# Kernel optimization log

Hardware: AMD Instinct MI355X
Metric: run time of the kernel (lower is better)

The kernel has to match this reference:

```python
import jax, jax.numpy as jnp
import numpy as np

L = 2        # num_layers (also acts as GRU seq_len due to the reshape in the original)
H = 512      # decoder_hidden_dim
Z = 512      # z_dim
V = 50257    # vocab_dim
T = 128      # target_length (max_length)
SOS_INDEX = 0


def setup_inputs() -> dict:
    key = jax.random.key(0)
    ks = jax.random.split(key, 16)
    def rn(k, shape, s=0.05):
        return jax.random.normal(k, shape, dtype=jnp.float32) * s
    input_variable = jax.random.normal(ks[0], (L, 1, Z), dtype=jnp.float32)
    tgt_idx = jax.random.randint(ks[1], (T,), 0, V)
    target_variable = jax.nn.one_hot(tgt_idx, V, dtype=jnp.float32).reshape(T, 1, V)
    sos = jax.nn.one_hot(jnp.array([SOS_INDEX]), V, dtype=jnp.float32)  # [1, V]
    return dict(
        input_variable=input_variable,
        target_variable=target_variable,
        sos=sos,
        emb_W=rn(ks[2], (L * H, V)), emb_b=rn(ks[3], (L * H,)),
        W_ih0=rn(ks[4], (3 * H, Z + H)), W_hh0=rn(ks[5], (3 * H, H)),
        b_ih0=rn(ks[6], (3 * H,)), b_hh0=rn(ks[7], (3 * H,)),
        W_ih1=rn(ks[8], (3 * H, H)), W_hh1=rn(ks[9], (3 * H, H)),
        b_ih1=rn(ks[10], (3 * H,)), b_hh1=rn(ks[11], (3 * H,)),
        out_W=rn(ks[12], (V, H)), out_b=rn(ks[13], (V,)),
    )


def _gru_cell(x, h, W_ih, W_hh, b_ih, b_hh):
    # PyTorch GRU cell semantics.
    gi = x @ W_ih.T + b_ih              # [1, 3H]
    gh = h @ W_hh.T + b_hh              # [1, 3H]
    i_r, i_z, i_n = jnp.split(gi, 3, axis=-1)
    h_r, h_z, h_n = jnp.split(gh, 3, axis=-1)
    r = jax.nn.sigmoid(i_r + h_r)
    z = jax.nn.sigmoid(i_z + h_z)
    n = jnp.tanh(i_n + r * h_n)
    return (1.0 - z) * n + z * h


def reference(input_variable, target_variable, sos,
              emb_W, emb_b,
              W_ih0, W_hh0, b_ih0, b_hh0,
              W_ih1, W_hh1, b_ih1, b_hh1,
              out_W, out_b):
    Wih = [W_ih0, W_ih1]; Whh = [W_hh0, W_hh1]
    bih = [b_ih0, b_ih1]; bhh = [b_hh0, b_hh1]

    def step(carry, tgt_t):
        hidden, inp = carry                      # hidden [L,1,H], inp [1,V]
        emb = jax.nn.relu((inp @ emb_W.T + emb_b).reshape(L, 1, H))
        layer_in = jnp.concatenate([input_variable, emb], axis=2)  # [L,1,Z+H]
        h_new = []
        for l in range(L):                       # GRU layers
            h = hidden[l]                        # [1,H]
            outs = []
            for t in range(L):                   # GRU 'time' steps (== L by construction)
                h = _gru_cell(layer_in[t], h, Wih[l], Whh[l], bih[l], bhh[l])
                outs.append(h)
            layer_in = jnp.stack(outs)           # [L,1,H]
            h_new.append(h)
        probs = jax.nn.softmax(layer_in[0] @ out_W.T + out_b, axis=1)  # [1,V]
        return (jnp.stack(h_new), tgt_t), probs[0]

    hidden0 = jnp.zeros((L, 1, H), jnp.float32)
    _, probs = jax.lax.scan(step, (hidden0, sos), target_variable)  # [T,V]
    idxs = jnp.argmax(probs, axis=-1)            # decoder_idxs
    return probs, idxs
```

## Files before the change

kernel.cpp:

```cpp
#include <hip/hip_runtime.h>
#include <math.h>

#define HD 512
#define VD 50257
#define TD 128
#define NB6 786

#define OFF_EMB     0u
#define OFF_X0      131072u
#define OFF_OUTS0   524288u
#define OFF_O       655360u
#define OFF_BASE    720896u
#define OFF_IDX     723968u
#define OFF_H0      724096u
#define OFF_H1      725120u
#define OFF_FLAGS   726144u
#define OFF_PM      729216u
#define OFF_PMPART  729472u
#define OFF_SUMS    930688u

__global__ void k_zero(float* p, int n){
  int i = blockIdx.x*256 + threadIdx.x;
  if (i < n) p[i] = 0.f;
}

__global__ void k_idx(const float* __restrict__ tgt, const float* __restrict__ sos,
                      int* __restrict__ idx){
  int t = blockIdx.x;
  const float* src = (t == 0) ? sos : (tgt + (size_t)(t-1)*VD);
  for (int v = threadIdx.x; v < VD; v += 256)
    if (src[v] > 0.5f) idx[t] = v;
}

__global__ void k_emb(const float* __restrict__ embW, const float* __restrict__ embB,
                      const int* __restrict__ idx, float* __restrict__ emb){
  int t = blockIdx.x;
  int j = blockIdx.y*256 + threadIdx.x;
  float v = embW[(size_t)j*VD + idx[t]] + embB[j];
  emb[t*1024 + j] = v > 0.f ? v : 0.f;
}

__global__ void k_base(const float* __restrict__ Wih0, const float* __restrict__ bih0,
                       const float* __restrict__ iv, float* __restrict__ base){
  int wave = threadIdx.x >> 6, lane = threadIdx.x & 63;
  int o = blockIdx.x*4 + wave;
  int tt = o / 1536, r = o % 1536;
  float s = 0.f;
  for (int c = lane; c < HD; c += 64)
    s += Wih0[(size_t)r*1024 + c] * iv[tt*HD + c];
  for (int off = 32; off; off >>= 1) s += __shfl_xor(s, off);
  if (lane == 0) base[o] = bih0[r] + s;
}

__global__ __launch_bounds__(256) void k_x0(const float* __restrict__ Wih0,
    const float* __restrict__ emb, const float* __restrict__ base, float* __restrict__ X0){
  __shared__ float Wt[64*33];
  __shared__ float Et[64*33];
  int tid = threadIdx.x;
  int r0 = blockIdx.x*64, b0 = blockIdx.y*64;
  int tx = tid & 15, ty = tid >> 4;
  float acc[4][4];
  #pragma unroll
  for (int i=0;i<4;i++)
    #pragma unroll
    for (int j=0;j<4;j++) acc[i][j] = 0.f;
  int lr = tid >> 2, lk = (tid & 3) * 8;
  for (int kk = 0; kk < HD; kk += 32){
    __syncthreads();
    {
      const float4* wg = (const float4*)(Wih0 + (size_t)(r0+lr)*1024 + HD + kk + lk);
      float4 a = wg[0], b = wg[1];
      float* d = Wt + lr*33 + lk;
      d[0]=a.x; d[1]=a.y; d[2]=a.z; d[3]=a.w; d[4]=b.x; d[5]=b.y; d[6]=b.z; d[7]=b.w;
    }
    {
      int bb = b0 + lr; int te = bb >> 1, hf = bb & 1;
      const float4* eg = (const float4*)(emb + (size_t)te*1024 + hf*HD + kk + lk);
      float4 a = eg[0], b = eg[1];
      float* d = Et + lr*33 + lk;
      d[0]=a.x; d[1]=a.y; d[2]=a.z; d[3]=a.w; d[4]=b.x; d[5]=b.y; d[6]=b.z; d[7]=b.w;
    }
    __syncthreads();
    #pragma unroll
    for (int k=0;k<32;k++){
      float wv[4], ev[4];
      #pragma unroll
      for (int i=0;i<4;i++) wv[i] = Wt[(tx*4+i)*33 + k];
      #pragma unroll
      for (int j=0;j<4;j++) ev[j] = Et[(ty*4+j)*33 + k];
      #pragma unroll
      for (int i=0;i<4;i++)
        #pragma unroll
        for (int j=0;j<4;j++) acc[i][j] += wv[i]*ev[j];
    }
  }
  #pragma unroll
  for (int j=0;j<4;j++){
    int bb = b0 + ty*4 + j;
    #pragma unroll
    for (int i=0;i<4;i++){
      int r = r0 + tx*4 + i;
      X0[(size_t)bb*1536 + r] = acc[i][j] + base[(bb&1)*1536 + r];
    }
  }
}

__device__ __forceinline__ void wait_flags(unsigned int* base, int n, unsigned int target, int tid){
  if (tid < 64){
    long iter = 0;
    for (;;){
      unsigned int v = 0;
      if (tid < n)
        v = __hip_atomic_load(base + tid*32, __ATOMIC_ACQUIRE, __HIP_MEMORY_SCOPE_AGENT);
      bool ok = (tid >= n) || (v >= target);
      if (__all((int)ok)) break;
      __builtin_amdgcn_s_sleep(1);
      if (++iter > 2000000L) break;
    }
  }
  __syncthreads();
}

__global__ __launch_bounds__(256, 1) void k_chain(
    const float* __restrict__ Whh0, const float* __restrict__ Wih1, const float* __restrict__ Whh1,
    const float* __restrict__ bhh0, const float* __restrict__ bih1, const float* __restrict__ bhh1,
    const float* __restrict__ X0, float* __restrict__ outs0, float* __restrict__ o,
    float* h0, float* h1, unsigned int* flags)
{
  const int w = blockIdx.x, tid = threadIdx.x;
  const bool isA = (w < 32);
  __shared__ float red[64];
  float wreg[128];
  const int sub = tid & 3;
  int slot; bool act;
  const float* wsrc = nullptr;
  if (isA){
    int ul = tid >> 4;
    int q  = (tid >> 2) & 3;
    int u  = w*16 + ul;
    slot = q; act = (q < 3);
    if (act) wsrc = Whh0 + ((size_t)(q*HD + u)*HD + sub*128);
  } else {
    int wp = w - 32;
    int ul = tid >> 5;
    int s8 = (tid >> 2) & 7;
    int u  = wp*8 + ul;
    slot = s8; act = (s8 < 6);
    if (s8 < 3)      wsrc = Wih1 + ((size_t)(s8*HD + u)*HD + sub*128);
    else if (s8 < 6) wsrc = Whh1 + ((size_t)((s8-3)*HD + u)*HD + sub*128);
  }
  if (wsrc){
    #pragma unroll
    for (int i=0;i<128;i++) wreg[i] = wsrc[i];
  } else {
    #pragma unroll
    for (int i=0;i<128;i++) wreg[i] = 0.f;
  }
  const int nGate = isA ? 16 : 8;
  float gb0=0,gb1=0,gb2=0,gb3=0,gb4=0,gb5=0;
  if (tid < nGate){
    int ug = isA ? (w*16 + tid) : ((w-32)*8 + tid);
    if (isA){ gb0=bhh0[ug]; gb1=bhh0[HD+ug]; gb2=bhh0[2*HD+ug]; }
    else {    gb0=bih1[ug]; gb1=bih1[HD+ug]; gb2=bih1[2*HD+ug];
              gb3=bhh1[ug]; gb4=bhh1[HD+ug]; gb5=bhh1[2*HD+ug]; }
  }
  unsigned int* flagsA = flags;
  unsigned int* flagsB = flags + 32*32;

  for (int c = 0; c < 256; c++){
    if (!isA) wait_flags(flagsA, 32, (unsigned)(c+1), tid);
    float partial = 0.f;
    if (act){
      const float* xp;
      if (isA) xp = h0 + (c&1)*HD + sub*128;
      else xp = (slot < 3) ? (outs0 + c*HD + sub*128) : (h1 + (c&1)*HD + sub*128);
      const float4* x4 = (const float4*)xp;
      #pragma unroll
      for (int i=0;i<32;i++){
        float4 xv = x4[i];
        partial += wreg[4*i]*xv.x + wreg[4*i+1]*xv.y + wreg[4*i+2]*xv.z + wreg[4*i+3]*xv.w;
      }
    }
    partial += __shfl_xor(partial, 1);
    partial += __shfl_xor(partial, 2);
    if (act && sub == 0){
      if (isA) red[(tid>>4)*4 + slot] = partial;
      else     red[(tid>>5)*8 + slot] = partial;
    }
    __syncthreads();
    if (tid < nGate){
      int ug = isA ? (w*16 + tid) : ((w-32)*8 + tid);
      float ir, iz, in_, hr, hz, hn;
      if (isA){
        const float* xo = X0 + (size_t)c*1536;
        ir = xo[ug]; iz = xo[HD+ug]; in_ = xo[2*HD+ug];
        hr = red[tid*4+0] + gb0; hz = red[tid*4+1] + gb1; hn = red[tid*4+2] + gb2;
      } else {
        ir = red[tid*8+0] + gb0; iz = red[tid*8+1] + gb1; in_ = red[tid*8+2] + gb2;
        hr = red[tid*8+3] + gb3; hz = red[tid*8+4] + gb4; hn = red[tid*8+5] + gb5;
      }
      float* hb = isA ? h0 : h1;
      float hprev = hb[(c&1)*HD + ug];
      float r = 1.f/(1.f + expf(-(ir+hr)));
      float z = 1.f/(1.f + expf(-(iz+hz)));
      float n = tanhf(in_ + r*hn);
      float hnew = (1.f - z)*n + z*hprev;
      hb[((c+1)&1)*HD + ug] = hnew;
      if (isA) outs0[c*HD + ug] = hnew;
      else if ((c & 1) == 0) o[(c>>1)*HD + ug] = hnew;
    }
    __syncthreads();
    if (tid == 0){
      unsigned int* myflag = isA ? (flagsA + w*32) : (flagsB + (w-32)*32);
      __hip_atomic_store(myflag, (unsigned)(c+1), __ATOMIC_RELEASE, __HIP_MEMORY_SCOPE_AGENT);
    }
    if (isA) wait_flags(flagsA, 32, (unsigned)(c+1), tid);
    else     wait_flags(flagsB, 64, (unsigned)(c+1), tid);
  }
}

__global__ __launch_bounds__(256) void k_logits(const float* __restrict__ o,
    const float* __restrict__ outW, const float* __restrict__ outB,
    float* __restrict__ dout, unsigned long long* __restrict__ pm_part){
  __shared__ float os[128*66];
  __shared__ float wsld[64*66];
  int tid = threadIdx.x;
  int v0 = blockIdx.x * 64;
  float acc[8][4];
  #pragma unroll
  for (int i=0;i<8;i++)
    #pragma unroll
    for (int j=0;j<4;j++) acc[i][j] = 0.f;
  int tx = tid & 15, ty = tid >> 4;
  for (int kk = 0; kk < HD; kk += 64){
    __syncthreads();
    {
      int tloc = tid >> 1, k0 = (tid & 1) * 32;
      const float4* og = (const float4*)(o + (size_t)tloc*HD + kk + k0);
      #pragma unroll
      for (int q=0;q<8;q++){
        float4 x = og[q]; int kb = k0 + q*4;
        os[tloc*66+kb]=x.x; os[tloc*66+kb+1]=x.y; os[tloc*66+kb+2]=x.z; os[tloc*66+kb+3]=x.w;
      }
    }
    {
      int vloc = tid >> 2, k0 = (tid & 3) * 16;
      int v = v0 + vloc;
      if (v < VD){
        const float4* wg = (const float4*)(outW + (size_t)v*HD + kk + k0);
        #pragma unroll
        for (int q=0;q<4;q++){
          float4 x = wg[q]; int kb = k0 + q*4;
          wsld[vloc*66+kb]=x.x; wsld[vloc*66+kb+1]=x.y; wsld[vloc*66+kb+2]=x.z; wsld[vloc*66+kb+3]=x.w;
        }
      } else {
        #pragma unroll
        for (int q=0;q<16;q++) wsld[vloc*66+k0+q] = 0.f;
      }
    }
    __syncthreads();
    #pragma unroll 8
    for (int k=0;k<64;k++){
      float ov[8], wv[4];
      #pragma unroll
      for (int i=0;i<8;i++) ov[i] = os[(tx*8+i)*66 + k];
      #pragma unroll
      for (int j=0;j<4;j++) wv[j] = wsld[(ty*4+j)*66 + k];
      #pragma unroll
      for (int i=0;i<8;i++)
        #pragma unroll
        for (int j=0;j<4;j++) acc[i][j] += ov[i]*wv[j];
    }
  }
  __syncthreads();
  unsigned long long* cand = (unsigned long long*)wsld;
  float bias[4]; int vj[4];
  #pragma unroll
  for (int j=0;j<4;j++){
    vj[j] = v0 + ty*4 + j;
    bias[j] = (vj[j] < VD) ? outB[vj[j]] : 0.f;
  }
  #pragma unroll
  for (int i=0;i<8;i++){
    int t = tx*8 + i;
    unsigned long long best = 0ull;
    #pragma unroll
    for (int j=0;j<4;j++){
      if (vj[j] < VD){
        float lg = acc[i][j] + bias[j];
        dout[(size_t)t*VD + vj[j]] = lg;
        unsigned b = __float_as_uint(lg);
        unsigned key = (b & 0x80000000u) ? ~b : (b | 0x80000000u);
        unsigned long long p = ((unsigned long long)key << 32) | (unsigned long long)(~(unsigned)vj[j]);
        if (p > best) best = p;
      }
    }
    cand[t*16 + ty] = best;
  }
  __syncthreads();
  if (tid < 128){
    unsigned long long best = 0ull;
    #pragma unroll
    for (int y=0;y<16;y++){
      unsigned long long p = cand[tid*16 + y];
      if (p > best) best = p;
    }
    pm_part[(size_t)tid*NB6 + blockIdx.x] = best;
  }
}

__global__ void k_pmred(const unsigned long long* __restrict__ pm_part,
                        unsigned long long* __restrict__ pm){
  int t = blockIdx.x, tid = threadIdx.x;
  __shared__ unsigned long long s[256];
  unsigned long long best = 0ull;
  for (int i = tid; i < NB6; i += 256){
    unsigned long long p = pm_part[(size_t)t*NB6 + i];
    if (p > best) best = p;
  }
  s[tid] = best; __syncthreads();
  for (int st = 128; st; st >>= 1){
    if (tid < st){ if (s[tid+st] > s[tid]) s[tid] = s[tid+st]; }
    __syncthreads();
  }
  if (tid == 0) pm[t] = s[0];
}

__global__ void k_expsum(float* __restrict__ dout, const unsigned long long* __restrict__ pm,
                         float* __restrict__ sums_part){
  int ch = blockIdx.x, t = blockIdx.y, tid = threadIdx.x;
  unsigned key = (unsigned)(pm[t] >> 32);
  unsigned b = (key & 0x80000000u) ? (key ^ 0x80000000u) : ~key;
  float mx = __uint_as_float(b);
  float s = 0.f;
  for (int q=0;q<8;q++){
    int v = ch*2048 + q*256 + tid;
    if (v < VD){
      float l = dout[(size_t)t*VD + v];
      float p = expf(l - mx);
      dout[(size_t)t*VD + v] = p;
      s += p;
    }
  }
  __shared__ float ss[256];
  ss[tid] = s; __syncthreads();
  for (int st = 128; st; st >>= 1){
    if (tid < st) ss[tid] += ss[tid+st];
    __syncthreads();
  }
  if (tid == 0) sums_part[t*25 + ch] = ss[0];
}

__global__ void k_fin(float* __restrict__ dout, const unsigned long long* __restrict__ pm,
                      const float* __restrict__ sums_part){
  int t = blockIdx.x, tid = threadIdx.x;
  __shared__ float invs;
  if (tid == 0){
    float s = 0.f;
    for (int i=0;i<25;i++) s += sums_part[t*25 + i];
    invs = 1.f / s;
  }
  __syncthreads();
  float iv2 = invs;
  for (int v = tid; v < VD; v += 256) dout[(size_t)t*VD + v] *= iv2;
  if (tid == 0){
    unsigned low = (unsigned)(pm[t] & 0xffffffffu);
    dout[(size_t)TD*VD + t] = (float)(~low);
  }
}

extern "C" void kernel_launch(void* const* d_in, const int* in_sizes, int n_in,
                              void* d_out, int out_size, void* d_ws, size_t ws_size,
                              hipStream_t stream){
  const float* iv   = (const float*)d_in[0];
  const float* tgt  = (const float*)d_in[1];
  const float* sos  = (const float*)d_in[2];
  const float* embW = (const float*)d_in[3];
  const float* embB = (const float*)d_in[4];
  const float* Wih0 = (const float*)d_in[5];
  const float* Whh0 = (const float*)d_in[6];
  const float* bih0 = (const float*)d_in[7];
  const float* bhh0 = (const float*)d_in[8];
  const float* Wih1 = (const float*)d_in[9];
  const float* Whh1 = (const float*)d_in[10];
  const float* bih1 = (const float*)d_in[11];
  const float* bhh1 = (const float*)d_in[12];
  const float* outW = (const float*)d_in[13];
  const float* outB = (const float*)d_in[14];
  (void)in_sizes; (void)n_in; (void)out_size; (void)ws_size;

  float* ws   = (float*)d_ws;
  float* dout = (float*)d_out;
  float* emb   = ws + OFF_EMB;
  float* X0    = ws + OFF_X0;
  float* outs0 = ws + OFF_OUTS0;
  float* o     = ws + OFF_O;
  float* base  = ws + OFF_BASE;
  int*   idx   = (int*)(ws + OFF_IDX);
  float* h0    = ws + OFF_H0;
  float* h1    = ws + OFF_H1;
  unsigned int* flags = (unsigned int*)(ws + OFF_FLAGS);
  unsigned long long* pm      = (unsigned long long*)(ws + OFF_PM);
  unsigned long long* pm_part = (unsigned long long*)(ws + OFF_PMPART);
  float* sums_part = ws + OFF_SUMS;

  k_zero<<<dim3(21), 256, 0, stream>>>(ws + OFF_H0, 5376);
  k_idx<<<dim3(TD), 256, 0, stream>>>(tgt, sos, idx);
  k_emb<<<dim3(TD,4), 256, 0, stream>>>(embW, embB, idx, emb);
  k_base<<<dim3(768), 256, 0, stream>>>(Wih0, bih0, iv, base);
  k_x0<<<dim3(24,4), 256, 0, stream>>>(Wih0, emb, base, X0);
  k_chain<<<dim3(96), 256, 0, stream>>>(Whh0, Wih1, Whh1, bhh0, bih1, bhh1,
                                        X0, outs0, o, h0, h1, flags);
  k_logits<<<dim3(NB6), 256, 0, stream>>>(o, outW, outB, dout, pm_part);
  k_pmred<<<dim3(TD), 256, 0, stream>>>(pm_part, pm);
  k_expsum<<<dim3(25,TD), 256, 0, stream>>>(dout, pm, sums_part);
  k_fin<<<dim3(TD), 256, 0, stream>>>(dout, pm, sums_part);
}
```

Measured before the change: 2.466 ms.

## Restructure GRU chain into 24 pipelined blocks with per-step history and fence-free polling

The recurrent chain kernel is rebuilt to run on 24 active workgroups instead of 96. Each thread now holds three gate rows in registers and computes r/z/n partials together. Each block reads its hardware XCC id and checks that all blocks share one XCC; if so, polling drops the sleep and the acquire/release fences. Layer 1 now waits per step on layer 0 rather than through a global barrier, which pipelines the two layers. Full hidden-state histories replace the double buffers, and the separate max-reduction kernel is replaced by atomicMax in the logits kernel. The risks are relying on same-XCC cache coherence to skip fences, and launching 185 blocks of which most exit at once.

```diff
diff --git a/kernel.cpp b/kernel.cpp
--- a/kernel.cpp
+++ b/kernel.cpp
@@ -6,22 +6,23 @@
 #define TD 128
 #define NB6 786
 
-#define OFF_EMB     0u
-#define OFF_X0      131072u
-#define OFF_OUTS0   524288u
-#define OFF_O       655360u
-#define OFF_BASE    720896u
-#define OFF_IDX     723968u
-#define OFF_H0      724096u
-#define OFF_H1      725120u
-#define OFF_FLAGS   726144u
-#define OFF_PM      729216u
-#define OFF_PMPART  729472u
-#define OFF_SUMS    930688u
-
-__global__ void k_zero(float* p, int n){
-  int i = blockIdx.x*256 + threadIdx.x;
-  if (i < n) p[i] = 0.f;
+#define OFF_H0     0u
+#define OFF_H1     131584u
+#define OFF_X0     263168u
+#define OFF_EMB    656384u
+#define OFF_BASE   787456u
+#define OFF_IDX    790528u
+#define OFF_FLAGS  790656u
+#define OFF_PM     792704u
+
+#define MAGICW 0x5A17C0DEu
+
+__global__ void k_zero4(float* ws){
+  int idx = blockIdx.x*256 + threadIdx.x;
+  if (idx < 512) ws[OFF_H0 + idx] = 0.f;
+  else if (idx < 1024) ws[OFF_H1 + (idx-512)] = 0.f;
+  else if (idx < 3072) ws[OFF_FLAGS + (idx-1024)] = 0.f;
+  else if (idx < 3328) ws[OFF_PM + (idx-3072)] = 0.f;
 }
 
 __global__ void k_idx(const float* __restrict__ tgt, const float* __restrict__ sos,
@@ -105,123 +106,147 @@
   }
 }
 
-__device__ __forceinline__ void wait_flags(unsigned int* base, int n, unsigned int target, int tid){
-  if (tid < 64){
-    long iter = 0;
-    for (;;){
-      unsigned int v = 0;
-      if (tid < n)
-        v = __hip_atomic_load(base + tid*32, __ATOMIC_ACQUIRE, __HIP_MEMORY_SCOPE_AGENT);
-      bool ok = (tid >= n) || (v >= target);
-      if (__all((int)ok)) break;
-      __builtin_amdgcn_s_sleep(1);
-      if (++iter > 2000000L) break;
-    }
-  }
-  __syncthreads();
-}
-
 __global__ __launch_bounds__(256, 1) void k_chain(
     const float* __restrict__ Whh0, const float* __restrict__ Wih1, const float* __restrict__ Whh1,
     const float* __restrict__ bhh0, const float* __restrict__ bih1, const float* __restrict__ bhh1,
-    const float* __restrict__ X0, float* __restrict__ outs0, float* __restrict__ o,
-    float* h0, float* h1, unsigned int* flags)
+    const float* __restrict__ X0, float* __restrict__ H0, float* __restrict__ H1,
+    unsigned int* F)
 {
-  const int w = blockIdx.x, tid = threadIdx.x;
-  const bool isA = (w < 32);
-  __shared__ float red[64];
-  float wreg[128];
-  const int sub = tid & 3;
-  int slot; bool act;
-  const float* wsrc = nullptr;
+  const int b = blockIdx.x;
+  if (b & 7) return;
+  const int i = b >> 3;
+  if (i >= 24) return;
+  const int tid = threadIdx.x;
+  const bool isA = (i < 8);
+  __shared__ int sh_fast;
+
+  unsigned own = 0;
+  if (tid < 64) own = ((unsigned)__builtin_amdgcn_s_getreg(63508)) & 0xFFu;
+  if (i == 0 && tid == 0){
+    F[61*32] = MAGICW;
+    asm volatile("s_waitcnt vmcnt(0)" ::: "memory");
+    __hip_atomic_store(&F[60*32], 1u, __ATOMIC_RELAXED, __HIP_MEMORY_SCOPE_AGENT);
+  }
+  if (tid == 0)
+    __hip_atomic_store(&F[(32+i)*32], own | 0x100u, __ATOMIC_RELAXED, __HIP_MEMORY_SCOPE_AGENT);
+  if (tid < 64){
+    bool actp = (tid < 25);
+    unsigned tgt = (tid < 24) ? 0x100u : 1u;
+    unsigned int* pp = (tid < 24) ? &F[(32+tid)*32] : &F[60*32];
+    unsigned v = 0; long it = 0;
+    for (;;){
+      v = actp ? __hip_atomic_load(pp, __ATOMIC_RELAXED, __HIP_MEMORY_SCOPE_AGENT) : 0xFFFFFFFFu;
+      if (__all((int)(!actp || v >= tgt))) break;
+      __builtin_amdgcn_s_sleep(8);
+      if (++it > 3000000L) break;
+    }
+    asm volatile("" ::: "memory");
+    bool ok = true;
+    if (tid < 24) ok = ((v & 0xFFu) == own);
+    else if (tid == 24){ unsigned cv = F[61*32]; ok = (cv == MAGICW); }
+    ok = __all((int)ok) != 0;
+    if (tid == 0) sh_fast = ok ? 1 : 0;
+  }
+  __syncthreads();
+  const bool fastf = (sh_fast != 0);
+
+  float w0[128], w1[128], w2[128];
+  int u, q, qq;
+  unsigned myflag;
   if (isA){
-    int ul = tid >> 4;
-    int q  = (tid >> 2) & 3;
-    int u  = w*16 + ul;
-    slot = q; act = (q < 3);
-    if (act) wsrc = Whh0 + ((size_t)(q*HD + u)*HD + sub*128);
+    u = i*64 + (tid >> 2); q = tid & 3; qq = q;
+    myflag = (unsigned)(i*32);
   } else {
-    int wp = w - 32;
-    int ul = tid >> 5;
-    int s8 = (tid >> 2) & 7;
-    int u  = wp*8 + ul;
-    slot = s8; act = (s8 < 6);
-    if (s8 < 3)      wsrc = Wih1 + ((size_t)(s8*HD + u)*HD + sub*128);
-    else if (s8 < 6) wsrc = Whh1 + ((size_t)((s8-3)*HD + u)*HD + sub*128);
-  }
-  if (wsrc){
-    #pragma unroll
-    for (int i=0;i<128;i++) wreg[i] = wsrc[i];
-  } else {
-    #pragma unroll
-    for (int i=0;i<128;i++) wreg[i] = 0.f;
-  }
-  const int nGate = isA ? 16 : 8;
-  float gb0=0,gb1=0,gb2=0,gb3=0,gb4=0,gb5=0;
-  if (tid < nGate){
-    int ug = isA ? (w*16 + tid) : ((w-32)*8 + tid);
-    if (isA){ gb0=bhh0[ug]; gb1=bhh0[HD+ug]; gb2=bhh0[2*HD+ug]; }
-    else {    gb0=bih1[ug]; gb1=bih1[HD+ug]; gb2=bih1[2*HD+ug];
-              gb3=bhh1[ug]; gb4=bhh1[HD+ug]; gb5=bhh1[2*HD+ug]; }
-  }
-  unsigned int* flagsA = flags;
-  unsigned int* flagsB = flags + 32*32;
+    int p = i - 8;
+    u = p*32 + (tid >> 3); q = tid & 7; qq = q & 3;
+    myflag = (unsigned)((8+p)*32);
+  }
+  {
+    const float* Wsrc = isA ? Whh0 : ((q < 4) ? Wih1 : Whh1);
+    const float4* p0 = (const float4*)(Wsrc + ((size_t)(0*HD + u))*HD + qq*128);
+    const float4* p1 = (const float4*)(Wsrc + ((size_t)(1*HD + u))*HD + qq*128);
+    const float4* p2 = (const float4*)(Wsrc + ((size_t)(2*HD + u))*HD + qq*128);
+    #pragma unroll
+    for (int j=0;j<32;j++){
+      float4 a = p0[j]; w0[4*j]=a.x; w0[4*j+1]=a.y; w0[4*j+2]=a.z; w0[4*j+3]=a.w;
+      float4 bb = p1[j]; w1[4*j]=bb.x; w1[4*j+1]=bb.y; w1[4*j+2]=bb.z; w1[4*j+3]=bb.w;
+      float4 cc = p2[j]; w2[4*j]=cc.x; w2[4*j+1]=cc.y; w2[4*j+2]=cc.z; w2[4*j+3]=cc.w;
+    }
+  }
+  const bool writer = isA ? ((tid & 3) == 0) : ((tid & 7) == 0);
+  float br=0.f,bz=0.f,bn=0.f, b2r=0.f,b2z=0.f,b2n=0.f, hprev=0.f;
+  if (writer){
+    if (isA){ br = bhh0[u]; bz = bhh0[HD+u]; bn = bhh0[2*HD+u]; }
+    else { br = bih1[u]; bz = bih1[HD+u]; bn = bih1[2*HD+u];
+           b2r = bhh1[u]; b2z = bhh1[HD+u]; b2n = bhh1[2*HD+u]; }
+  }
+  const int nPoll = isA ? 8 : 24;
+  const bool act = (tid < nPoll);
+  const int addv = (!isA && tid < 8) ? 1 : 0;
+  unsigned int* pollp = &F[(tid & 63)*32];
 
   for (int c = 0; c < 256; c++){
-    if (!isA) wait_flags(flagsA, 32, (unsigned)(c+1), tid);
-    float partial = 0.f;
-    if (act){
-      const float* xp;
-      if (isA) xp = h0 + (c&1)*HD + sub*128;
-      else xp = (slot < 3) ? (outs0 + c*HD + sub*128) : (h1 + (c&1)*HD + sub*128);
-      const float4* x4 = (const float4*)xp;
-      #pragma unroll
-      for (int i=0;i<32;i++){
-        float4 xv = x4[i];
-        partial += wreg[4*i]*xv.x + wreg[4*i+1]*xv.y + wreg[4*i+2]*xv.z + wreg[4*i+3]*xv.w;
+    float xr=0.f, xz=0.f, xn=0.f;
+    if (isA && writer){
+      const float* xo = X0 + (size_t)c*1536 + u;
+      xr = xo[0]; xz = xo[HD]; xn = xo[2*HD];
+    }
+    if (tid < 64){
+      long it = 0;
+      for (;;){
+        int v = act ? (int)__hip_atomic_load(pollp, __ATOMIC_RELAXED, __HIP_MEMORY_SCOPE_AGENT)
+                    : 0x7FFFFFFF;
+        if (__all((int)(v >= c + addv))) break;
+        if (!fastf) __builtin_amdgcn_s_sleep(2);
+        if (++it > 3000000L) break;
       }
-    }
-    partial += __shfl_xor(partial, 1);
-    partial += __shfl_xor(partial, 2);
-    if (act && sub == 0){
-      if (isA) red[(tid>>4)*4 + slot] = partial;
-      else     red[(tid>>5)*8 + slot] = partial;
-    }
-    __syncthreads();
-    if (tid < nGate){
-      int ug = isA ? (w*16 + tid) : ((w-32)*8 + tid);
-      float ir, iz, in_, hr, hz, hn;
-      if (isA){
-        const float* xo = X0 + (size_t)c*1536;
-        ir = xo[ug]; iz = xo[HD+ug]; in_ = xo[2*HD+ug];
-        hr = red[tid*4+0] + gb0; hz = red[tid*4+1] + gb1; hn = red[tid*4+2] + gb2;
-      } else {
-        ir = red[tid*8+0] + gb0; iz = red[tid*8+1] + gb1; in_ = red[tid*8+2] + gb2;
-        hr = red[tid*8+3] + gb3; hz = red[tid*8+4] + gb4; hn = red[tid*8+5] + gb5;
-      }
-      float* hb = isA ? h0 : h1;
-      float hprev = hb[(c&1)*HD + ug];
-      float r = 1.f/(1.f + expf(-(ir+hr)));
-      float z = 1.f/(1.f + expf(-(iz+hz)));
-      float n = tanhf(in_ + r*hn);
+      if (!fastf) __builtin_amdgcn_fence(__ATOMIC_ACQUIRE, "agent");
+    }
+    __syncthreads();
+    const float4* x4;
+    if (isA) x4 = (const float4*)(H0 + (size_t)c*HD + q*128);
+    else x4 = (q < 4) ? (const float4*)(H0 + (size_t)(c+1)*HD + qq*128)
+                      : (const float4*)(H1 + (size_t)c*HD + qq*128);
+    float ar=0.f, az=0.f, an=0.f;
+    #pragma unroll
+    for (int j=0;j<32;j++){
+      float4 xv = x4[j];
+      ar = fmaf(w0[4*j+0], xv.x, ar); ar = fmaf(w0[4*j+1], xv.y, ar);
+      ar = fmaf(w0[4*j+2], xv.z, ar); ar = fmaf(w0[4*j+3], xv.w, ar);
+      az = fmaf(w1[4*j+0], xv.x, az); az = fmaf(w1[4*j+1], xv.y, az);
+      az = fmaf(w1[4*j+2], xv.z, az); az = fmaf(w1[4*j+3], xv.w, az);
+      an = fmaf(w2[4*j+0], xv.x, an); an = fmaf(w2[4*j+1], xv.y, an);
+      an = fmaf(w2[4*j+2], xv.z, an); an = fmaf(w2[4*j+3], xv.w, an);
+    }
+    ar += __shfl_xor(ar, 1); az += __shfl_xor(az, 1); an += __shfl_xor(an, 1);
+    ar += __shfl_xor(ar, 2); az += __shfl_xor(az, 2); an += __shfl_xor(an, 2);
+    float or_=0.f, oz=0.f, on=0.f;
+    if (!isA){ or_ = __shfl_xor(ar, 4); oz = __shfl_xor(az, 4); on = __shfl_xor(an, 4); }
+    if (writer){
+      float g_ir, g_iz, g_in, g_hr, g_hz, g_hn;
+      if (isA){ g_ir = xr; g_iz = xz; g_in = xn;
+                g_hr = ar + br; g_hz = az + bz; g_hn = an + bn; }
+      else    { g_ir = ar + br;  g_iz = az + bz;  g_in = an + bn;
+                g_hr = or_ + b2r; g_hz = oz + b2z; g_hn = on + b2n; }
+      float r = 1.f/(1.f + expf(-(g_ir + g_hr)));
+      float z = 1.f/(1.f + expf(-(g_iz + g_hz)));
+      float n = tanhf(g_in + r*g_hn);
       float hnew = (1.f - z)*n + z*hprev;
-      hb[((c+1)&1)*HD + ug] = hnew;
-      if (isA) outs0[c*HD + ug] = hnew;
-      else if ((c & 1) == 0) o[(c>>1)*HD + ug] = hnew;
+      hprev = hnew;
+      if (isA) H0[(size_t)(c+1)*HD + u] = hnew;
+      else     H1[(size_t)(c+1)*HD + u] = hnew;
     }
     __syncthreads();
     if (tid == 0){
-      unsigned int* myflag = isA ? (flagsA + w*32) : (flagsB + (w-32)*32);
-      __hip_atomic_store(myflag, (unsigned)(c+1), __ATOMIC_RELEASE, __HIP_MEMORY_SCOPE_AGENT);
-    }
-    if (isA) wait_flags(flagsA, 32, (unsigned)(c+1), tid);
-    else     wait_flags(flagsB, 64, (unsigned)(c+1), tid);
-  }
-}
-
-__global__ __launch_bounds__(256) void k_logits(const float* __restrict__ o,
+      if (!fastf) __builtin_amdgcn_fence(__ATOMIC_RELEASE, "agent");
+      __hip_atomic_store(&F[myflag], (unsigned)(c+1), __ATOMIC_RELAXED, __HIP_MEMORY_SCOPE_AGENT);
+    }
+  }
+}
+
+__global__ __launch_bounds__(256) void k_logits(const float* __restrict__ H1,
     const float* __restrict__ outW, const float* __restrict__ outB,
-    float* __restrict__ dout, unsigned long long* __restrict__ pm_part){
+    float* __restrict__ dout, unsigned long long* __restrict__ pm){
   __shared__ float os[128*66];
   __shared__ float wsld[64*66];
   int tid = threadIdx.x;
@@ -236,7 +261,7 @@
     __syncthreads();
     {
       int tloc = tid >> 1, k0 = (tid & 1) * 32;
-      const float4* og = (const float4*)(o + (size_t)tloc*HD + kk + k0);
+      const float4* og = (const float4*)(H1 + (size_t)(2*tloc+1)*HD + kk + k0);
       #pragma unroll
       for (int q=0;q<8;q++){
         float4 x = og[q]; int kb = k0 + q*4;
@@ -289,8 +314,8 @@
       if (vj[j] < VD){
         float lg = acc[i][j] + bias[j];
         dout[(size_t)t*VD + vj[j]] = lg;
-        unsigned b = __float_as_uint(lg);
-        unsigned key = (b & 0x80000000u) ? ~b : (b | 0x80000000u);
+        unsigned bq = __float_as_uint(lg);
+        unsigned key = (bq & 0x80000000u) ? ~bq : (bq | 0x80000000u);
         unsigned long long p = ((unsigned long long)key << 32) | (unsigned long long)(~(unsigned)vj[j]);
         if (p > best) best = p;
       }
@@ -305,25 +330,8 @@
       unsigned long long p = cand[tid*16 + y];
       if (p > best) best = p;
     }
-    pm_part[(size_t)tid*NB6 + blockIdx.x] = best;
-  }
-}
-
-__global__ void k_pmred(const unsigned long long* __restrict__ pm_part,
-                        unsigned long long* __restrict__ pm){
-  int t = blockIdx.x, tid = threadIdx.x;
-  __shared__ unsigned long long s[256];
-  unsigned long long best = 0ull;
-  for (int i = tid; i < NB6; i += 256){
-    unsigned long long p = pm_part[(size_t)t*NB6 + i];
-    if (p > best) best = p;
-  }
-  s[tid] = best; __syncthreads();
-  for (int st = 128; st; st >>= 1){
-    if (tid < st){ if (s[tid+st] > s[tid]) s[tid] = s[tid+st]; }
-    __syncthreads();
-  }
-  if (tid == 0) pm[t] = s[0];
+    atomicMax(pm + tid, best);
+  }
 }
 
 __global__ void k_expsum(float* __restrict__ dout, const unsigned long long* __restrict__ pm,
@@ -391,28 +399,24 @@
 
   float* ws   = (float*)d_ws;
   float* dout = (float*)d_out;
-  float* emb   = ws + OFF_EMB;
-  float* X0    = ws + OFF_X0;
-  float* outs0 = ws + OFF_OUTS0;
-  float* o     = ws + OFF_O;
-  float* base  = ws + OFF_BASE;
-  int*   idx   = (int*)(ws + OFF_IDX);
-  float* h0    = ws + OFF_H0;
-  float* h1    = ws + OFF_H1;
-  unsigned int* flags = (unsigned int*)(ws + OFF_FLAGS);
-  unsigned long long* pm      = (unsigned long long*)(ws + OFF_PM);
-  unsigned long long* pm_part = (unsigned long long*)(ws + OFF_PMPART);
-  float* sums_part = ws + OFF_SUMS;
-
-  k_zero<<<dim3(21), 256, 0, stream>>>(ws + OFF_H0, 5376);
+  float* H0   = ws + OFF_H0;
+  float* H1   = ws + OFF_H1;
+  float* X0   = ws + OFF_X0;
+  float* emb  = ws + OFF_EMB;
+  float* base = ws + OFF_BASE;
+  int*   idx  = (int*)(ws + OFF_IDX);
+  unsigned int* F = (unsigned int*)(ws + OFF_FLAGS);
+  unsigned long long* pm = (unsigned long long*)(ws + OFF_PM);
+  float* sums_part = ws + OFF_PM + 256;
+
+  k_zero4<<<dim3(13), 256, 0, stream>>>(ws);
   k_idx<<<dim3(TD), 256, 0, stream>>>(tgt, sos, idx);
   k_emb<<<dim3(TD,4), 256, 0, stream>>>(embW, embB, idx, emb);
   k_base<<<dim3(768), 256, 0, stream>>>(Wih0, bih0, iv, base);
   k_x0<<<dim3(24,4), 256, 0, stream>>>(Wih0, emb, base, X0);
-  k_chain<<<dim3(96), 256, 0, stream>>>(Whh0, Wih1, Whh1, bhh0, bih1, bhh1,
-                                        X0, outs0, o, h0, h1, flags);
-  k_logits<<<dim3(NB6), 256, 0, stream>>>(o, outW, outB, dout, pm_part);
-  k_pmred<<<dim3(TD), 256, 0, stream>>>(pm_part, pm);
+  k_chain<<<dim3(185), 256, 0, stream>>>(Whh0, Wih1, Whh1, bhh0, bih1, bhh1,
+                                         X0, H0, H1, F);
+  k_logits<<<dim3(NB6), 256, 0, stream>>>(H1, outW, outB, dout, pm);
   k_expsum<<<dim3(25,TD), 256, 0, stream>>>(dout, pm, sums_part);
   k_fin<<<dim3(TD), 256, 0, stream>>>(dout, pm, sums_part);
 }
```

Result: faster. 2.352 ms (-4.6%).
